# Performance work log

Measured on AMD Instinct MI355X. Metric: run time of the kernel, lower is better.

## Reference

```python
import jax, jax.numpy as jnp
import numpy as np

V, T, NS, NH, E, H = 4, 4, 100000, 12288, 100000, 64
NEG_SLOPE = 0.01  # nn.LeakyReLU default


def setup_inputs() -> dict:
    key = jax.random.key(0)
    k1, k2, k3, k4, k5 = jax.random.split(key, 5)
    x = jax.random.normal(k1, (V, T, NS), dtype=jnp.float32)          # per-var, per-t scalar node features
    src_idx = jax.random.randint(k2, (V, T, E), 0, NS, dtype=jnp.int32)
    dst_idx = jax.random.randint(k3, (V, T, E), 0, NH, dtype=jnp.int32)
    W = jax.random.normal(k4, (V, T, H), dtype=jnp.float32)            # GraphConv weight, in_feats=1 -> [1,H] per etype
    b = jax.random.normal(k5, (V, T, H), dtype=jnp.float32) * 0.02     # GraphConv bias per etype
    return {"x": x, "W": W, "b": b, "src_idx": src_idx, "dst_idx": dst_idx, "n_healpix": NH}


def reference(x, W, b, src_idx, dst_idx, n_healpix):
    # x: [V,T,NS]; W,b: [V,T,H]; src_idx,dst_idx: [V,T,E]
    x = jnp.nan_to_num(x, nan=0.0)

    def conv_scalar(x_v, src, dst):
        # x_v: [T,NS] (all timestep features for this var), src/dst: [E] for ONE edge type
        ones = jnp.ones(src.shape, x_v.dtype)
        deg_out = jax.ops.segment_sum(ones, src, num_segments=NS)       # out-degree of src nodes
        deg_in = jax.ops.segment_sum(ones, dst, num_segments=n_healpix)  # in-degree of dst nodes
        norm_src = jax.lax.rsqrt(jnp.maximum(deg_out, 1.0))
        norm_dst = jax.lax.rsqrt(jnp.maximum(deg_in, 1.0))
        msg = x_v[:, src] * norm_src[src]                                # [T,E] gather
        agg = jax.vmap(lambda m: jax.ops.segment_sum(m, dst, num_segments=n_healpix))(msg)  # [T,NH]
        return agg * norm_dst                                            # norm='both'

    # HeteroGraphConv bug-faithful: for each var, EVERY per-t' conv is applied to each x[:,t]
    # s[v, t', t, n] = normalized scatter of x[v,t] through edges of etype t'
    s = jax.vmap(lambda xv, sv, dv: jax.vmap(lambda se, de: conv_scalar(xv, se, de))(sv, dv))(
        x, src_idx, dst_idx)                                             # [V,T',T,NH]

    # in_feats=1: linear is outer product with W row; bias + LeakyReLU inside each conv, sum over etypes t'
    h = jax.nn.leaky_relu(s[..., None] * W[:, :, None, None, :] + b[:, :, None, None, :],
                          negative_slope=NEG_SLOPE)                      # [V,T',T,NH,H]
    out = h.sum(axis=1)                                                  # aggregate='sum' over edge types -> [V,T,NH,H]
    # final stacking: stack over t (dim=1) then over vars (dim=1) -> [NH, V, T, H]
    return jnp.transpose(out, (2, 0, 1, 3))
```

## Files before the change

kernel.cpp:

```cpp
#include <hip/hip_runtime.h>
#include <math.h>

#define V    4
#define T    4
#define NSRC 100000
#define NHX  12288
#define E    100000
#define H    64
#define VT   16

#define SL    16
#define SLE   (E/SL)
#define HF    4
#define HE    (E/HF)
#define CW    (NSRC/8)
#define LDSW  12500
#define NCH   12
#define NPB   8

#define S1_TRANS  391
#define S1_CNT    (HF*VT)
#define S1_DHIST  (SL*VT)
#define S2_SCAN   (NCH*VT)
#define S2_NSFIN  ((VT*CW + 1023)/1024)

typedef float vf4 __attribute__((ext_vector_type(4)));

__global__ void __launch_bounds__(1024)
s1_kernel(const float* __restrict__ x, const int* __restrict__ src,
          const int* __restrict__ dst, float4* __restrict__ x4,
          unsigned int* __restrict__ cnt_part, unsigned char* __restrict__ ph8,
          unsigned int* __restrict__ cs) {
    __shared__ unsigned int lds[LDSW];
    const int b = blockIdx.x, tid = threadIdx.x;

    if (b < S1_TRANS) {
        const int g = b * 1024 + tid;
        if (g < V * NSRC) {
            const int v = g / NSRC, s = g - v * NSRC;
            const float* xr = x + (size_t)v * T * NSRC + s;
            float a0 = xr[0], a1 = xr[NSRC], a2 = xr[2 * NSRC], a3 = xr[3 * NSRC];
            float4 r;
            r.x = (a0 == a0) ? a0 : 0.0f;
            r.y = (a1 == a1) ? a1 : 0.0f;
            r.z = (a2 == a2) ? a2 : 0.0f;
            r.w = (a3 == a3) ? a3 : 0.0f;
            x4[g] = r;
        }
        return;
    }
    if (b < S1_TRANS + S1_CNT) {
        const int idx = b - S1_TRANS;
        const int hf = idx & 3;
        const int vt = idx >> 2;
        for (int i = tid; i < CW; i += 1024) lds[i] = 0u;
        __syncthreads();
        const int* s_row = src + vt * E + hf * HE;
        for (int e = tid; e < HE; e += 1024) {
            const unsigned r = (unsigned)s_row[e];
            atomicAdd(&lds[r >> 3], 1u << ((r & 7) * 4));
        }
        __syncthreads();
        unsigned int* outp = cnt_part + ((size_t)hf * VT + vt) * CW;
        for (int i = tid; i < CW; i += 1024) outp[i] = lds[i];
        return;
    }
    {
        const int idx = b - (S1_TRANS + S1_CNT);
        const int sl = idx & 15, vt = idx >> 4;
        for (int i = tid; i < NHX; i += 1024) lds[i] = 0u;
        __syncthreads();
        const int* d_row = dst + vt * E + sl * SLE;
        for (int e = tid; e < SLE; e += 1024)
            atomicAdd(&lds[d_row[e]], 1u);
        __syncthreads();
        unsigned char* outp = ph8 + ((size_t)vt * SL + sl) * NHX;
        for (int i = tid; i < NHX; i += 1024)
            outp[i] = (unsigned char)lds[i];
        const int lane = tid & 63, wv = tid >> 6;
        if (wv < NCH) {
            unsigned int s = 0;
#pragma unroll
            for (int i = 0; i < 16; ++i) s += lds[wv * 1024 + i * 64 + lane];
#pragma unroll
            for (int off = 32; off > 0; off >>= 1)
                s += (unsigned int)__shfl_down((int)s, off, 64);
            if (lane == 0) cs[((size_t)vt * SL + sl) * NCH + wv] = s;
        }
    }
}

__global__ void __launch_bounds__(1024)
s2_kernel(const unsigned int* __restrict__ cnt_part,
          const unsigned char* __restrict__ ph8,
          const unsigned int* __restrict__ cs,
          unsigned char* __restrict__ deg8,
          unsigned char* __restrict__ pre8,
          unsigned int* __restrict__ colstart) {
    const int b = blockIdx.x, tid = threadIdx.x;

    if (b < S2_SCAN) {
        const int vt = b & 15, ch = b >> 4;
        const int lane = tid & 63, wv = tid >> 6;
        const int d = ch * 1024 + tid;
        __shared__ unsigned int wsum[16];
        __shared__ unsigned int sbase;
        if (wv == 0) {
            unsigned int p = 0;
            if (lane < SL)
                for (int c = 0; c < ch; ++c)
                    p += cs[((size_t)vt * SL + lane) * NCH + c];
#pragma unroll
            for (int off = 8; off > 0; off >>= 1)
                p += (unsigned int)__shfl_down((int)p, off, 64);
            if (lane == 0) sbase = p;
        }
        unsigned int h[SL];
        unsigned int tot = 0;
#pragma unroll
        for (int s = 0; s < SL; ++s) {
            h[s] = (unsigned int)ph8[((size_t)vt * SL + s) * NHX + d];
            tot += h[s];
        }
        unsigned int incl = tot;
#pragma unroll
        for (int off = 1; off < 64; off <<= 1) {
            const unsigned int vup = (unsigned int)__shfl_up((int)incl, off, 64);
            if (lane >= off) incl += vup;
        }
        if (lane == 63) wsum[wv] = incl;
        __syncthreads();
        if (tid == 0) {
            unsigned int run = sbase;
#pragma unroll
            for (int w = 0; w < 16; ++w) { const unsigned int t2 = wsum[w]; wsum[w] = run; run += t2; }
        }
        __syncthreads();
        const unsigned int excl = wsum[wv] + (incl - tot);
        const size_t vd = (size_t)vt * NHX + d;
        colstart[vd] = excl | (tot << 20);
        unsigned int acc = 0;
#pragma unroll
        for (int s = 0; s < SL; ++s) {
            pre8[((size_t)vt * SL + s) * NHX + d] = (unsigned char)acc;
            acc += h[s];
        }
        return;
    }
    {
        const int g = (b - S2_SCAN) * 1024 + tid;
        if (g >= VT * CW) return;
        unsigned slo = 0, shi = 0;
#pragma unroll
        for (int hf = 0; hf < HF; ++hf) {
            const unsigned w = cnt_part[(size_t)hf * (VT * CW) + g];
            slo += w & 0x0F0F0F0Fu;
            shi += (w >> 4) & 0x0F0F0F0Fu;
        }
        uint2 o;
        o.x = (slo & 0xFFu) | ((shi & 0xFFu) << 8) |
              (((slo >> 8) & 0xFFu) << 16) | (((shi >> 8) & 0xFFu) << 24);
        o.y = ((slo >> 16) & 0xFFu) | (((shi >> 16) & 0xFFu) << 8) |
              (((slo >> 24) & 0xFFu) << 16) | ((shi >> 24) << 24);
        *(uint2*)(deg8 + 8 * (size_t)g) = o;
    }
}

__global__ void __launch_bounds__(1024)
s3_reorder(const int* __restrict__ src, const int* __restrict__ dst,
           const unsigned int* __restrict__ colstart,
           const unsigned char* __restrict__ pre8,
           int* __restrict__ sorted) {
    const int b = blockIdx.x;
    const int k = b & 7, j = b >> 3;
    const int vt = 2 * k + (j & 1);
    const int sl = j >> 1;
    __shared__ unsigned int pos[NHX];
    const unsigned int*  cst = colstart + (size_t)vt * NHX;
    const unsigned char* pr  = pre8 + ((size_t)vt * SL + sl) * NHX;
    for (int i = threadIdx.x; i < NHX; i += 1024)
        pos[i] = (cst[i] & 0xFFFFFu) + (unsigned int)pr[i];
    __syncthreads();
    const int* s_row = src + vt * E + sl * SLE;
    const int* d_row = dst + vt * E + sl * SLE;
    int* outp = sorted + (size_t)vt * E;
    for (int e = threadIdx.x; e < SLE; e += 1024) {
        const int d = d_row[e];
        const int s = s_row[e];
        const unsigned int p = atomicAdd(&pos[d], 1u);
        outp[p] = s;
    }
}

__global__ void __launch_bounds__(256)
s4_accum(const float4* __restrict__ x4, const int* __restrict__ sorted,
         const unsigned char* __restrict__ deg8,
         const unsigned int* __restrict__ colstart,
         float4* __restrict__ sval) {
    const int b = blockIdx.x;
    const int k = b & 7, j = b >> 3;
    const int vt = 2 * k + (j & 1);
    const int chunk = j >> 1;
    const int d = chunk * 64 + (threadIdx.x >> 2);
    const int q = threadIdx.x & 3;
    const int v = vt >> 2;
    const size_t vd = (size_t)vt * NHX + d;
    const unsigned int pk   = colstart[vd];
    const unsigned int base = pk & 0xFFFFFu;
    const unsigned int deg  = pk >> 20;
    const int*           srt = sorted + (size_t)vt * E;
    const unsigned char* dg  = deg8 + (size_t)vt * NSRC;
    const float4*      x_row = x4 + (size_t)v * NSRC;
    float4 acc = make_float4(0.f, 0.f, 0.f, 0.f);
    for (unsigned int i = q; i < deg; i += 4) {
        const int s = srt[base + i];
        const float4 xa = x_row[s];
        const float  na = rsqrtf(fmaxf((float)dg[s], 1.0f));
        acc.x += xa.x * na; acc.y += xa.y * na;
        acc.z += xa.z * na; acc.w += xa.w * na;
    }
    acc.x += __shfl_xor(acc.x, 1, 64);
    acc.y += __shfl_xor(acc.y, 1, 64);
    acc.z += __shfl_xor(acc.z, 1, 64);
    acc.w += __shfl_xor(acc.w, 1, 64);
    acc.x += __shfl_xor(acc.x, 2, 64);
    acc.y += __shfl_xor(acc.y, 2, 64);
    acc.z += __shfl_xor(acc.z, 2, 64);
    acc.w += __shfl_xor(acc.w, 2, 64);
    if (q == 0) {
        const float nd = rsqrtf(fmaxf((float)deg, 1.0f));
        acc.x *= nd; acc.y *= nd; acc.z *= nd; acc.w *= nd;
        sval[vd] = acc;
    }
}

__global__ void __launch_bounds__(256)
s5_epilogue(const float4* __restrict__ sval, const float* __restrict__ Wm,
            const float* __restrict__ bm, float* __restrict__ out) {
    const int n0  = blockIdx.x * NPB;
    const int tid = threadIdx.x;
    __shared__ float sW[VT * H];
    __shared__ float sb[VT * H];
    __shared__ float sv[VT][T][NPB];

    for (int i = tid; i < VT * H; i += 256) { sW[i] = Wm[i]; sb[i] = bm[i]; }
    if (tid < VT * NPB) {
        const int vt = tid >> 3, n = tid & 7;
        const float4 r = sval[(size_t)vt * NHX + n0 + n];
        sv[vt][0][n] = r.x; sv[vt][1][n] = r.y;
        sv[vt][2][n] = r.z; sv[vt][3][n] = r.w;
    }
    __syncthreads();

    const int v  = tid >> 6;
    const int t  = (tid >> 4) & 3;
    const int hb = (tid & 15) * 4;
    float4 Wr[4], Br[4];
#pragma unroll
    for (int tp = 0; tp < 4; ++tp) {
        const int wi = (v * 4 + tp) * H + hb;
        Wr[tp] = *(const float4*)&sW[wi];
        Br[tp] = *(const float4*)&sb[wi];
    }
#pragma unroll
    for (int n = 0; n < NPB; ++n) {
        float4 o = make_float4(0.f, 0.f, 0.f, 0.f);
#pragma unroll
        for (int tp = 0; tp < 4; ++tp) {
            const float s = sv[v * 4 + tp][t][n];
            float a;
            a = fmaf(s, Wr[tp].x, Br[tp].x); o.x += (a > 0.f) ? a : 0.01f * a;
            a = fmaf(s, Wr[tp].y, Br[tp].y); o.y += (a > 0.f) ? a : 0.01f * a;
            a = fmaf(s, Wr[tp].z, Br[tp].z); o.z += (a > 0.f) ? a : 0.01f * a;
            a = fmaf(s, Wr[tp].w, Br[tp].w); o.w += (a > 0.f) ? a : 0.01f * a;
        }
        vf4* dstp = (vf4*)(out + (size_t)(n0 + n) * (V * T * H)) + tid;
        __builtin_nontemporal_store(*(vf4*)&o, dstp);
    }
}

extern "C" void kernel_launch(void* const* d_in, const int* in_sizes, int n_in,
                              void* d_out, int out_size, void* d_ws, size_t ws_size,
                              hipStream_t stream) {
    const float* x   = (const float*)d_in[0];
    const float* Wm  = (const float*)d_in[1];
    const float* bm  = (const float*)d_in[2];
    const int*   src = (const int*)d_in[3];
    const int*   dst = (const int*)d_in[4];
    float* out = (float*)d_out;

    char* ws = (char*)d_ws;
    size_t off = 0;
    float4* x4 = (float4*)(ws + off);                   off += (size_t)V * NSRC * 16;
    float4* sval = (float4*)(ws + off);                 off += (size_t)VT * NHX * 16;
    unsigned char* deg8 = (unsigned char*)(ws + off);   off += (size_t)VT * NSRC;
    unsigned char* ph8 = (unsigned char*)(ws + off);    off += (size_t)VT * SL * NHX;
    unsigned char* pre8 = (unsigned char*)(ws + off);   off += (size_t)VT * SL * NHX;
    unsigned int* colstart = (unsigned int*)(ws + off); off += (size_t)VT * NHX * 4;
    unsigned int* cs = (unsigned int*)(ws + off);       off += (size_t)VT * SL * NCH * 4;
    unsigned int* cnt_part = (unsigned int*)(ws + off); off += (size_t)HF * VT * CW * 4;
    int* sorted = (int*)(ws + off);                     off += (size_t)VT * E * 4;

    s1_kernel<<<S1_TRANS + S1_CNT + S1_DHIST, 1024, 0, stream>>>(
        x, src, dst, x4, cnt_part, ph8, cs);
    s2_kernel<<<S2_SCAN + S2_NSFIN, 1024, 0, stream>>>(
        cnt_part, ph8, cs, deg8, pre8, colstart);
    s3_reorder<<<SL * VT, 1024, 0, stream>>>(src, dst, colstart, pre8, sorted);
    s4_accum<<<3072, 256, 0, stream>>>(x4, sorted, deg8, colstart, sval);
    s5_epilogue<<<NHX / NPB, 256, 0, stream>>>(sval, Wm, bm, out);
}
```

Before: 141.4 us.

## Replace counting-sort CSR gather with direct global float atomics scatter

After: 428.7 us. 203% more time.

```diff
diff --git a/kernel.cpp b/kernel.cpp
--- a/kernel.cpp
+++ b/kernel.cpp
@@ -9,32 +9,30 @@
 #define H    64
 #define VT   16
 
-#define SL    16
-#define SLE   (E/SL)
-#define HF    4
-#define HE    (E/HF)
 #define CW    (NSRC/8)
 #define LDSW  12500
-#define NCH   12
 #define NPB   8
 
-#define S1_TRANS  391
-#define S1_CNT    (HF*VT)
-#define S1_DHIST  (SL*VT)
-#define S2_SCAN   (NCH*VT)
-#define S2_NSFIN  ((VT*CW + 1023)/1024)
+#define K1_TRANS  391
+#define K1_DOUT   VT
+#define K1_DIN    VT
+#define K1_ZERO   48
+#define K1_TOT    (K1_TRANS+K1_DOUT+K1_DIN+K1_ZERO)
+
+#define K2_BPV    100
+#define K2_EPB    (E/K2_BPV)
 
 typedef float vf4 __attribute__((ext_vector_type(4)));
 
 __global__ void __launch_bounds__(1024)
-s1_kernel(const float* __restrict__ x, const int* __restrict__ src,
-          const int* __restrict__ dst, float4* __restrict__ x4,
-          unsigned int* __restrict__ cnt_part, unsigned char* __restrict__ ph8,
-          unsigned int* __restrict__ cs) {
+k1_prep(const float* __restrict__ x, const int* __restrict__ src,
+        const int* __restrict__ dst, float4* __restrict__ x4,
+        unsigned char* __restrict__ deg8, unsigned char* __restrict__ degin8,
+        float4* __restrict__ sval) {
     __shared__ unsigned int lds[LDSW];
     const int b = blockIdx.x, tid = threadIdx.x;
 
-    if (b < S1_TRANS) {
+    if (b < K1_TRANS) {
         const int g = b * 1024 + tid;
         if (g < V * NSRC) {
             const int v = g / NSRC, s = g - v * NSRC;
@@ -49,194 +47,89 @@
         }
         return;
     }
-    if (b < S1_TRANS + S1_CNT) {
-        const int idx = b - S1_TRANS;
-        const int hf = idx & 3;
-        const int vt = idx >> 2;
+    if (b < K1_TRANS + K1_DOUT) {
+        const int vt = b - K1_TRANS;
         for (int i = tid; i < CW; i += 1024) lds[i] = 0u;
         __syncthreads();
-        const int* s_row = src + vt * E + hf * HE;
-        for (int e = tid; e < HE; e += 1024) {
-            const unsigned r = (unsigned)s_row[e];
-            atomicAdd(&lds[r >> 3], 1u << ((r & 7) * 4));
+        const int4* s_row = (const int4*)(src + vt * E);
+        for (int e = tid; e < E / 4; e += 1024) {
+            const int4 q = s_row[e];
+            atomicAdd(&lds[((unsigned)q.x) >> 3], 1u << ((q.x & 7) * 4));
+            atomicAdd(&lds[((unsigned)q.y) >> 3], 1u << ((q.y & 7) * 4));
+            atomicAdd(&lds[((unsigned)q.z) >> 3], 1u << ((q.z & 7) * 4));
+            atomicAdd(&lds[((unsigned)q.w) >> 3], 1u << ((q.w & 7) * 4));
         }
         __syncthreads();
-        unsigned int* outp = cnt_part + ((size_t)hf * VT + vt) * CW;
-        for (int i = tid; i < CW; i += 1024) outp[i] = lds[i];
+        unsigned char* outp = deg8 + (size_t)vt * NSRC;
+        for (int i = tid; i < CW; i += 1024) {
+            const unsigned w = lds[i];
+            uint2 o;
+            o.x = (w & 0xFu) | (((w >> 4) & 0xFu) << 8) |
+                  (((w >> 8) & 0xFu) << 16) | (((w >> 12) & 0xFu) << 24);
+            o.y = ((w >> 16) & 0xFu) | (((w >> 20) & 0xFu) << 8) |
+                  (((w >> 24) & 0xFu) << 16) | (((w >> 28) & 0xFu) << 24);
+            *(uint2*)(outp + 8 * (size_t)i) = o;
+        }
+        return;
+    }
+    if (b < K1_TRANS + K1_DOUT + K1_DIN) {
+        const int vt = b - (K1_TRANS + K1_DOUT);
+        for (int i = tid; i < NHX; i += 1024) lds[i] = 0u;
+        __syncthreads();
+        const int4* d_row = (const int4*)(dst + vt * E);
+        for (int e = tid; e < E / 4; e += 1024) {
+            const int4 q = d_row[e];
+            atomicAdd(&lds[q.x], 1u);
+            atomicAdd(&lds[q.y], 1u);
+            atomicAdd(&lds[q.z], 1u);
+            atomicAdd(&lds[q.w], 1u);
+        }
+        __syncthreads();
+        unsigned char* outp = degin8 + (size_t)vt * NHX;
+        for (int i = tid; i < NHX; i += 1024)
+            outp[i] = (unsigned char)lds[i];
         return;
     }
     {
-        const int idx = b - (S1_TRANS + S1_CNT);
-        const int sl = idx & 15, vt = idx >> 4;
-        for (int i = tid; i < NHX; i += 1024) lds[i] = 0u;
-        __syncthreads();
-        const int* d_row = dst + vt * E + sl * SLE;
-        for (int e = tid; e < SLE; e += 1024)
-            atomicAdd(&lds[d_row[e]], 1u);
-        __syncthreads();
-        unsigned char* outp = ph8 + ((size_t)vt * SL + sl) * NHX;
-        for (int i = tid; i < NHX; i += 1024)
-            outp[i] = (unsigned char)lds[i];
-        const int lane = tid & 63, wv = tid >> 6;
-        if (wv < NCH) {
-            unsigned int s = 0;
+        const int idx = b - (K1_TRANS + K1_DOUT + K1_DIN);
+        const float4 z = make_float4(0.f, 0.f, 0.f, 0.f);
+        float4* p = sval + (size_t)idx * 4096;
 #pragma unroll
-            for (int i = 0; i < 16; ++i) s += lds[wv * 1024 + i * 64 + lane];
-#pragma unroll
-            for (int off = 32; off > 0; off >>= 1)
-                s += (unsigned int)__shfl_down((int)s, off, 64);
-            if (lane == 0) cs[((size_t)vt * SL + sl) * NCH + wv] = s;
-        }
-    }
-}
-
-__global__ void __launch_bounds__(1024)
-s2_kernel(const unsigned int* __restrict__ cnt_part,
-          const unsigned char* __restrict__ ph8,
-          const unsigned int* __restrict__ cs,
-          unsigned char* __restrict__ deg8,
-          unsigned char* __restrict__ pre8,
-          unsigned int* __restrict__ colstart) {
-    const int b = blockIdx.x, tid = threadIdx.x;
-
-    if (b < S2_SCAN) {
-        const int vt = b & 15, ch = b >> 4;
-        const int lane = tid & 63, wv = tid >> 6;
-        const int d = ch * 1024 + tid;
-        __shared__ unsigned int wsum[16];
-        __shared__ unsigned int sbase;
-        if (wv == 0) {
-            unsigned int p = 0;
-            if (lane < SL)
-                for (int c = 0; c < ch; ++c)
-                    p += cs[((size_t)vt * SL + lane) * NCH + c];
-#pragma unroll
-            for (int off = 8; off > 0; off >>= 1)
-                p += (unsigned int)__shfl_down((int)p, off, 64);
-            if (lane == 0) sbase = p;
-        }
-        unsigned int h[SL];
-        unsigned int tot = 0;
-#pragma unroll
-        for (int s = 0; s < SL; ++s) {
-            h[s] = (unsigned int)ph8[((size_t)vt * SL + s) * NHX + d];
-            tot += h[s];
-        }
-        unsigned int incl = tot;
-#pragma unroll
-        for (int off = 1; off < 64; off <<= 1) {
-            const unsigned int vup = (unsigned int)__shfl_up((int)incl, off, 64);
-            if (lane >= off) incl += vup;
-        }
-        if (lane == 63) wsum[wv] = incl;
-        __syncthreads();
-        if (tid == 0) {
-            unsigned int run = sbase;
-#pragma unroll
-            for (int w = 0; w < 16; ++w) { const unsigned int t2 = wsum[w]; wsum[w] = run; run += t2; }
-        }
-        __syncthreads();
-        const unsigned int excl = wsum[wv] + (incl - tot);
-        const size_t vd = (size_t)vt * NHX + d;
-        colstart[vd] = excl | (tot << 20);
-        unsigned int acc = 0;
-#pragma unroll
-        for (int s = 0; s < SL; ++s) {
-            pre8[((size_t)vt * SL + s) * NHX + d] = (unsigned char)acc;
-            acc += h[s];
-        }
-        return;
-    }
-    {
-        const int g = (b - S2_SCAN) * 1024 + tid;
-        if (g >= VT * CW) return;
-        unsigned slo = 0, shi = 0;
-#pragma unroll
-        for (int hf = 0; hf < HF; ++hf) {
-            const unsigned w = cnt_part[(size_t)hf * (VT * CW) + g];
-            slo += w & 0x0F0F0F0Fu;
-            shi += (w >> 4) & 0x0F0F0F0Fu;
-        }
-        uint2 o;
-        o.x = (slo & 0xFFu) | ((shi & 0xFFu) << 8) |
-              (((slo >> 8) & 0xFFu) << 16) | (((shi >> 8) & 0xFFu) << 24);
-        o.y = ((slo >> 16) & 0xFFu) | (((shi >> 16) & 0xFFu) << 8) |
-              (((slo >> 24) & 0xFFu) << 16) | ((shi >> 24) << 24);
-        *(uint2*)(deg8 + 8 * (size_t)g) = o;
-    }
-}
-
-__global__ void __launch_bounds__(1024)
-s3_reorder(const int* __restrict__ src, const int* __restrict__ dst,
-           const unsigned int* __restrict__ colstart,
-           const unsigned char* __restrict__ pre8,
-           int* __restrict__ sorted) {
-    const int b = blockIdx.x;
-    const int k = b & 7, j = b >> 3;
-    const int vt = 2 * k + (j & 1);
-    const int sl = j >> 1;
-    __shared__ unsigned int pos[NHX];
-    const unsigned int*  cst = colstart + (size_t)vt * NHX;
-    const unsigned char* pr  = pre8 + ((size_t)vt * SL + sl) * NHX;
-    for (int i = threadIdx.x; i < NHX; i += 1024)
-        pos[i] = (cst[i] & 0xFFFFFu) + (unsigned int)pr[i];
-    __syncthreads();
-    const int* s_row = src + vt * E + sl * SLE;
-    const int* d_row = dst + vt * E + sl * SLE;
-    int* outp = sorted + (size_t)vt * E;
-    for (int e = threadIdx.x; e < SLE; e += 1024) {
-        const int d = d_row[e];
-        const int s = s_row[e];
-        const unsigned int p = atomicAdd(&pos[d], 1u);
-        outp[p] = s;
+        for (int c = 0; c < 4; ++c) p[tid + c * 1024] = z;
     }
 }
 
 __global__ void __launch_bounds__(256)
-s4_accum(const float4* __restrict__ x4, const int* __restrict__ sorted,
-         const unsigned char* __restrict__ deg8,
-         const unsigned int* __restrict__ colstart,
+k2_accum(const float4* __restrict__ x4, const int* __restrict__ src,
+         const int* __restrict__ dst, const unsigned char* __restrict__ deg8,
          float4* __restrict__ sval) {
     const int b = blockIdx.x;
     const int k = b & 7, j = b >> 3;
     const int vt = 2 * k + (j & 1);
-    const int chunk = j >> 1;
-    const int d = chunk * 64 + (threadIdx.x >> 2);
-    const int q = threadIdx.x & 3;
+    const int blk = j >> 1;
     const int v = vt >> 2;
-    const size_t vd = (size_t)vt * NHX + d;
-    const unsigned int pk   = colstart[vd];
-    const unsigned int base = pk & 0xFFFFFu;
-    const unsigned int deg  = pk >> 20;
-    const int*           srt = sorted + (size_t)vt * E;
-    const unsigned char* dg  = deg8 + (size_t)vt * NSRC;
-    const float4*      x_row = x4 + (size_t)v * NSRC;
-    float4 acc = make_float4(0.f, 0.f, 0.f, 0.f);
-    for (unsigned int i = q; i < deg; i += 4) {
-        const int s = srt[base + i];
+    const int* s_row = src + vt * E;
+    const int* d_row = dst + vt * E;
+    const unsigned char* dg = deg8 + (size_t)vt * NSRC;
+    const float4* x_row = x4 + (size_t)v * NSRC;
+    float* sv = (float*)(sval + (size_t)vt * NHX);
+    const int e0 = blk * K2_EPB;
+    for (int e = e0 + threadIdx.x; e < e0 + K2_EPB; e += 256) {
+        const int s = s_row[e];
+        const int d = d_row[e];
         const float4 xa = x_row[s];
         const float  na = rsqrtf(fmaxf((float)dg[s], 1.0f));
-        acc.x += xa.x * na; acc.y += xa.y * na;
-        acc.z += xa.z * na; acc.w += xa.w * na;
-    }
-    acc.x += __shfl_xor(acc.x, 1, 64);
-    acc.y += __shfl_xor(acc.y, 1, 64);
-    acc.z += __shfl_xor(acc.z, 1, 64);
-    acc.w += __shfl_xor(acc.w, 1, 64);
-    acc.x += __shfl_xor(acc.x, 2, 64);
-    acc.y += __shfl_xor(acc.y, 2, 64);
-    acc.z += __shfl_xor(acc.z, 2, 64);
-    acc.w += __shfl_xor(acc.w, 2, 64);
-    if (q == 0) {
-        const float nd = rsqrtf(fmaxf((float)deg, 1.0f));
-        acc.x *= nd; acc.y *= nd; acc.z *= nd; acc.w *= nd;
-        sval[vd] = acc;
+        atomicAdd(sv + 4 * d + 0, xa.x * na);
+        atomicAdd(sv + 4 * d + 1, xa.y * na);
+        atomicAdd(sv + 4 * d + 2, xa.z * na);
+        atomicAdd(sv + 4 * d + 3, xa.w * na);
     }
 }
 
 __global__ void __launch_bounds__(256)
-s5_epilogue(const float4* __restrict__ sval, const float* __restrict__ Wm,
-            const float* __restrict__ bm, float* __restrict__ out) {
+k3_epilogue(const float4* __restrict__ sval, const unsigned char* __restrict__ degin8,
+            const float* __restrict__ Wm, const float* __restrict__ bm,
+            float* __restrict__ out) {
     const int n0  = blockIdx.x * NPB;
     const int tid = threadIdx.x;
     __shared__ float sW[VT * H];
@@ -247,8 +140,9 @@
     if (tid < VT * NPB) {
         const int vt = tid >> 3, n = tid & 7;
         const float4 r = sval[(size_t)vt * NHX + n0 + n];
-        sv[vt][0][n] = r.x; sv[vt][1][n] = r.y;
-        sv[vt][2][n] = r.z; sv[vt][3][n] = r.w;
+        const float nd = rsqrtf(fmaxf((float)degin8[(size_t)vt * NHX + n0 + n], 1.0f));
+        sv[vt][0][n] = r.x * nd; sv[vt][1][n] = r.y * nd;
+        sv[vt][2][n] = r.z * nd; sv[vt][3][n] = r.w * nd;
     }
     __syncthreads();
 
@@ -291,21 +185,12 @@
 
     char* ws = (char*)d_ws;
     size_t off = 0;
-    float4* x4 = (float4*)(ws + off);                   off += (size_t)V * NSRC * 16;
-    float4* sval = (float4*)(ws + off);                 off += (size_t)VT * NHX * 16;
-    unsigned char* deg8 = (unsigned char*)(ws + off);   off += (size_t)VT * NSRC;
-    unsigned char* ph8 = (unsigned char*)(ws + off);    off += (size_t)VT * SL * NHX;
-    unsigned char* pre8 = (unsigned char*)(ws + off);   off += (size_t)VT * SL * NHX;
-    unsigned int* colstart = (unsigned int*)(ws + off); off += (size_t)VT * NHX * 4;
-    unsigned int* cs = (unsigned int*)(ws + off);       off += (size_t)VT * SL * NCH * 4;
-    unsigned int* cnt_part = (unsigned int*)(ws + off); off += (size_t)HF * VT * CW * 4;
-    int* sorted = (int*)(ws + off);                     off += (size_t)VT * E * 4;
+    float4* x4 = (float4*)(ws + off);                 off += (size_t)V * NSRC * 16;
+    float4* sval = (float4*)(ws + off);               off += (size_t)VT * NHX * 16;
+    unsigned char* deg8 = (unsigned char*)(ws + off); off += (size_t)VT * NSRC;
+    unsigned char* degin8 = (unsigned char*)(ws + off); off += (size_t)VT * NHX;
 
-    s1_kernel<<<S1_TRANS + S1_CNT + S1_DHIST, 1024, 0, stream>>>(
-        x, src, dst, x4, cnt_part, ph8, cs);
-    s2_kernel<<<S2_SCAN + S2_NSFIN, 1024, 0, stream>>>(
-        cnt_part, ph8, cs, deg8, pre8, colstart);
-    s3_reorder<<<SL * VT, 1024, 0, stream>>>(src, dst, colstart, pre8, sorted);
-    s4_accum<<<3072, 256, 0, stream>>>(x4, sorted, deg8, colstart, sval);
-    s5_epilogue<<<NHX / NPB, 256, 0, stream>>>(sval, Wm, bm, out);
+    k1_prep<<<K1_TOT, 1024, 0, stream>>>(x, src, dst, x4, deg8, degin8, sval);
+    k2_accum<<<8 * 2 * K2_BPV, 256, 0, stream>>>(x4, src, dst, deg8, sval);
+    k3_epilogue<<<NHX / NPB, 256, 0, stream>>>(sval, degin8, Wm, bm, out);
 }
```

## Pack source degree into sorted edge list and drop partial out-degree merge

Applied to the files above, without the earlier changes.

After: 139.8 us. No clear change (-1.1%).

```diff
diff --git a/kernel.cpp b/kernel.cpp
--- a/kernel.cpp
+++ b/kernel.cpp
@@ -11,25 +11,23 @@
 
 #define SL    16
 #define SLE   (E/SL)
-#define HF    4
-#define HE    (E/HF)
 #define CW    (NSRC/8)
 #define LDSW  12500
 #define NCH   12
 #define NPB   8
 
 #define S1_TRANS  391
-#define S1_CNT    (HF*VT)
+#define S1_DOUT   VT
 #define S1_DHIST  (SL*VT)
+#define S1_TOT    (S1_TRANS+S1_DOUT+S1_DHIST)
 #define S2_SCAN   (NCH*VT)
-#define S2_NSFIN  ((VT*CW + 1023)/1024)
 
 typedef float vf4 __attribute__((ext_vector_type(4)));
 
 __global__ void __launch_bounds__(1024)
 s1_kernel(const float* __restrict__ x, const int* __restrict__ src,
           const int* __restrict__ dst, float4* __restrict__ x4,
-          unsigned int* __restrict__ cnt_part, unsigned char* __restrict__ ph8,
+          unsigned char* __restrict__ deg8, unsigned char* __restrict__ ph8,
           unsigned int* __restrict__ cs) {
     __shared__ unsigned int lds[LDSW];
     const int b = blockIdx.x, tid = threadIdx.x;
@@ -49,24 +47,33 @@
         }
         return;
     }
-    if (b < S1_TRANS + S1_CNT) {
-        const int idx = b - S1_TRANS;
-        const int hf = idx & 3;
-        const int vt = idx >> 2;
+    if (b < S1_TRANS + S1_DOUT) {
+        const int vt = b - S1_TRANS;
         for (int i = tid; i < CW; i += 1024) lds[i] = 0u;
         __syncthreads();
-        const int* s_row = src + vt * E + hf * HE;
-        for (int e = tid; e < HE; e += 1024) {
-            const unsigned r = (unsigned)s_row[e];
-            atomicAdd(&lds[r >> 3], 1u << ((r & 7) * 4));
-        }
-        __syncthreads();
-        unsigned int* outp = cnt_part + ((size_t)hf * VT + vt) * CW;
-        for (int i = tid; i < CW; i += 1024) outp[i] = lds[i];
+        const int4* s_row = (const int4*)(src + vt * E);
+        for (int e = tid; e < E / 4; e += 1024) {
+            const int4 q = s_row[e];
+            atomicAdd(&lds[((unsigned)q.x) >> 3], 1u << ((q.x & 7) * 4));
+            atomicAdd(&lds[((unsigned)q.y) >> 3], 1u << ((q.y & 7) * 4));
+            atomicAdd(&lds[((unsigned)q.z) >> 3], 1u << ((q.z & 7) * 4));
+            atomicAdd(&lds[((unsigned)q.w) >> 3], 1u << ((q.w & 7) * 4));
+        }
+        __syncthreads();
+        unsigned char* outp = deg8 + (size_t)vt * NSRC;
+        for (int i = tid; i < CW; i += 1024) {
+            const unsigned w = lds[i];
+            uint2 o;
+            o.x = (w & 0xFu) | (((w >> 4) & 0xFu) << 8) |
+                  (((w >> 8) & 0xFu) << 16) | (((w >> 12) & 0xFu) << 24);
+            o.y = ((w >> 16) & 0xFu) | (((w >> 20) & 0xFu) << 8) |
+                  (((w >> 24) & 0xFu) << 16) | (((w >> 28) & 0xFu) << 24);
+            *(uint2*)(outp + 8 * (size_t)i) = o;
+        }
         return;
     }
     {
-        const int idx = b - (S1_TRANS + S1_CNT);
+        const int idx = b - (S1_TRANS + S1_DOUT);
         const int sl = idx & 15, vt = idx >> 4;
         for (int i = tid; i < NHX; i += 1024) lds[i] = 0u;
         __syncthreads();
@@ -91,78 +98,55 @@
 }
 
 __global__ void __launch_bounds__(1024)
-s2_kernel(const unsigned int* __restrict__ cnt_part,
-          const unsigned char* __restrict__ ph8,
+s2_kernel(const unsigned char* __restrict__ ph8,
           const unsigned int* __restrict__ cs,
-          unsigned char* __restrict__ deg8,
           unsigned char* __restrict__ pre8,
           unsigned int* __restrict__ colstart) {
     const int b = blockIdx.x, tid = threadIdx.x;
-
-    if (b < S2_SCAN) {
-        const int vt = b & 15, ch = b >> 4;
-        const int lane = tid & 63, wv = tid >> 6;
-        const int d = ch * 1024 + tid;
-        __shared__ unsigned int wsum[16];
-        __shared__ unsigned int sbase;
-        if (wv == 0) {
-            unsigned int p = 0;
-            if (lane < SL)
-                for (int c = 0; c < ch; ++c)
-                    p += cs[((size_t)vt * SL + lane) * NCH + c];
-#pragma unroll
-            for (int off = 8; off > 0; off >>= 1)
-                p += (unsigned int)__shfl_down((int)p, off, 64);
-            if (lane == 0) sbase = p;
-        }
-        unsigned int h[SL];
-        unsigned int tot = 0;
-#pragma unroll
-        for (int s = 0; s < SL; ++s) {
-            h[s] = (unsigned int)ph8[((size_t)vt * SL + s) * NHX + d];
-            tot += h[s];
-        }
-        unsigned int incl = tot;
-#pragma unroll
-        for (int off = 1; off < 64; off <<= 1) {
-            const unsigned int vup = (unsigned int)__shfl_up((int)incl, off, 64);
-            if (lane >= off) incl += vup;
-        }
-        if (lane == 63) wsum[wv] = incl;
-        __syncthreads();
-        if (tid == 0) {
-            unsigned int run = sbase;
-#pragma unroll
-            for (int w = 0; w < 16; ++w) { const unsigned int t2 = wsum[w]; wsum[w] = run; run += t2; }
-        }
-        __syncthreads();
-        const unsigned int excl = wsum[wv] + (incl - tot);
-        const size_t vd = (size_t)vt * NHX + d;
-        colstart[vd] = excl | (tot << 20);
-        unsigned int acc = 0;
-#pragma unroll
-        for (int s = 0; s < SL; ++s) {
-            pre8[((size_t)vt * SL + s) * NHX + d] = (unsigned char)acc;
-            acc += h[s];
-        }
-        return;
-    }
-    {
-        const int g = (b - S2_SCAN) * 1024 + tid;
-        if (g >= VT * CW) return;
-        unsigned slo = 0, shi = 0;
-#pragma unroll
-        for (int hf = 0; hf < HF; ++hf) {
-            const unsigned w = cnt_part[(size_t)hf * (VT * CW) + g];
-            slo += w & 0x0F0F0F0Fu;
-            shi += (w >> 4) & 0x0F0F0F0Fu;
-        }
-        uint2 o;
-        o.x = (slo & 0xFFu) | ((shi & 0xFFu) << 8) |
-              (((slo >> 8) & 0xFFu) << 16) | (((shi >> 8) & 0xFFu) << 24);
-        o.y = ((slo >> 16) & 0xFFu) | (((shi >> 16) & 0xFFu) << 8) |
-              (((slo >> 24) & 0xFFu) << 16) | ((shi >> 24) << 24);
-        *(uint2*)(deg8 + 8 * (size_t)g) = o;
+    const int vt = b & 15, ch = b >> 4;
+    const int lane = tid & 63, wv = tid >> 6;
+    const int d = ch * 1024 + tid;
+    __shared__ unsigned int wsum[16];
+    __shared__ unsigned int sbase;
+    if (wv == 0) {
+        unsigned int p = 0;
+        if (lane < SL)
+            for (int c = 0; c < ch; ++c)
+                p += cs[((size_t)vt * SL + lane) * NCH + c];
+#pragma unroll
+        for (int off = 8; off > 0; off >>= 1)
+            p += (unsigned int)__shfl_down((int)p, off, 64);
+        if (lane == 0) sbase = p;
+    }
+    unsigned int h[SL];
+    unsigned int tot = 0;
+#pragma unroll
+    for (int s = 0; s < SL; ++s) {
+        h[s] = (unsigned int)ph8[((size_t)vt * SL + s) * NHX + d];
+        tot += h[s];
+    }
+    unsigned int incl = tot;
+#pragma unroll
+    for (int off = 1; off < 64; off <<= 1) {
+        const unsigned int vup = (unsigned int)__shfl_up((int)incl, off, 64);
+        if (lane >= off) incl += vup;
+    }
+    if (lane == 63) wsum[wv] = incl;
+    __syncthreads();
+    if (tid == 0) {
+        unsigned int run = sbase;
+#pragma unroll
+        for (int w = 0; w < 16; ++w) { const unsigned int t2 = wsum[w]; wsum[w] = run; run += t2; }
+    }
+    __syncthreads();
+    const unsigned int excl = wsum[wv] + (incl - tot);
+    const size_t vd = (size_t)vt * NHX + d;
+    colstart[vd] = excl | (tot << 20);
+    unsigned int acc = 0;
+#pragma unroll
+    for (int s = 0; s < SL; ++s) {
+        pre8[((size_t)vt * SL + s) * NHX + d] = (unsigned char)acc;
+        acc += h[s];
     }
 }
 
@@ -170,7 +154,8 @@
 s3_reorder(const int* __restrict__ src, const int* __restrict__ dst,
            const unsigned int* __restrict__ colstart,
            const unsigned char* __restrict__ pre8,
-           int* __restrict__ sorted) {
+           const unsigned char* __restrict__ deg8,
+           unsigned int* __restrict__ sorted) {
     const int b = blockIdx.x;
     const int k = b & 7, j = b >> 3;
     const int vt = 2 * k + (j & 1);
@@ -183,18 +168,19 @@
     __syncthreads();
     const int* s_row = src + vt * E + sl * SLE;
     const int* d_row = dst + vt * E + sl * SLE;
-    int* outp = sorted + (size_t)vt * E;
+    const unsigned char* dg = deg8 + (size_t)vt * NSRC;
+    unsigned int* outp = sorted + (size_t)vt * E;
     for (int e = threadIdx.x; e < SLE; e += 1024) {
         const int d = d_row[e];
-        const int s = s_row[e];
+        const unsigned int s = (unsigned int)s_row[e];
+        const unsigned int w = s | ((unsigned int)dg[s] << 17);
         const unsigned int p = atomicAdd(&pos[d], 1u);
-        outp[p] = s;
+        outp[p] = w;
     }
 }
 
 __global__ void __launch_bounds__(256)
-s4_accum(const float4* __restrict__ x4, const int* __restrict__ sorted,
-         const unsigned char* __restrict__ deg8,
+s4_accum(const float4* __restrict__ x4, const unsigned int* __restrict__ sorted,
          const unsigned int* __restrict__ colstart,
          float4* __restrict__ sval) {
     const int b = blockIdx.x;
@@ -208,14 +194,14 @@
     const unsigned int pk   = colstart[vd];
     const unsigned int base = pk & 0xFFFFFu;
     const unsigned int deg  = pk >> 20;
-    const int*           srt = sorted + (size_t)vt * E;
-    const unsigned char* dg  = deg8 + (size_t)vt * NSRC;
-    const float4*      x_row = x4 + (size_t)v * NSRC;
+    const unsigned int* srt = sorted + (size_t)vt * E;
+    const float4*     x_row = x4 + (size_t)v * NSRC;
     float4 acc = make_float4(0.f, 0.f, 0.f, 0.f);
     for (unsigned int i = q; i < deg; i += 4) {
-        const int s = srt[base + i];
+        const unsigned int w = srt[base + i];
+        const int   s  = (int)(w & 0x1FFFFu);
+        const float na = rsqrtf(fmaxf((float)(w >> 17), 1.0f));
         const float4 xa = x_row[s];
-        const float  na = rsqrtf(fmaxf((float)dg[s], 1.0f));
         acc.x += xa.x * na; acc.y += xa.y * na;
         acc.z += xa.z * na; acc.w += xa.w * na;
     }
@@ -298,14 +284,11 @@
     unsigned char* pre8 = (unsigned char*)(ws + off);   off += (size_t)VT * SL * NHX;
     unsigned int* colstart = (unsigned int*)(ws + off); off += (size_t)VT * NHX * 4;
     unsigned int* cs = (unsigned int*)(ws + off);       off += (size_t)VT * SL * NCH * 4;
-    unsigned int* cnt_part = (unsigned int*)(ws + off); off += (size_t)HF * VT * CW * 4;
-    int* sorted = (int*)(ws + off);                     off += (size_t)VT * E * 4;
-
-    s1_kernel<<<S1_TRANS + S1_CNT + S1_DHIST, 1024, 0, stream>>>(
-        x, src, dst, x4, cnt_part, ph8, cs);
-    s2_kernel<<<S2_SCAN + S2_NSFIN, 1024, 0, stream>>>(
-        cnt_part, ph8, cs, deg8, pre8, colstart);
-    s3_reorder<<<SL * VT, 1024, 0, stream>>>(src, dst, colstart, pre8, sorted);
-    s4_accum<<<3072, 256, 0, stream>>>(x4, sorted, deg8, colstart, sval);
+    unsigned int* sorted = (unsigned int*)(ws + off);   off += (size_t)VT * E * 4;
+
+    s1_kernel<<<S1_TOT, 1024, 0, stream>>>(x, src, dst, x4, deg8, ph8, cs);
+    s2_kernel<<<S2_SCAN, 1024, 0, stream>>>(ph8, cs, pre8, colstart);
+    s3_reorder<<<SL * VT, 1024, 0, stream>>>(src, dst, colstart, pre8, deg8, sorted);
+    s4_accum<<<3072, 256, 0, stream>>>(x4, sorted, colstart, sval);
     s5_epilogue<<<NHX / NPB, 256, 0, stream>>>(sval, Wm, bm, out);
 }
```
